# Performance work log

Measured on AMD Instinct MI355X. Metric: run time of the kernel, lower is better.

The kernel has to match this reference:

```python
import jax, jax.numpy as jnp
import numpy as np

E = 1024   # embedding_dim
H = 16     # heads
W = 1024   # lag / seq length
B = 4      # batch
D = E // H # head dim


def setup_inputs() -> dict:
    key = jax.random.key(0)
    ks = jax.random.split(key, 5)
    scale = E ** -0.5
    return {
        "x":   jax.random.normal(ks[0], (3, B, E, W), dtype=jnp.float32),
        "L_Q": jax.random.normal(ks[1], (E, E), dtype=jnp.float32) * scale,
        "L_K": jax.random.normal(ks[2], (E, E), dtype=jnp.float32) * scale,
        "L_V": jax.random.normal(ks[3], (E, E), dtype=jnp.float32) * scale,
        "M":   jax.random.normal(ks[4], (E, E), dtype=jnp.float32) * (1.0 / (2 * E)) ** 0.5,
        "b":   jnp.zeros((E, 1), dtype=jnp.float32),
    }


def reference(x, L_Q, L_K, L_V, M, b):
    # x: [3, B, E, W] channels-first; x[0]=K input, x[1]=Q input, x[2]=V input
    K = jnp.einsum('ef,bfw->bew', L_K, x[0])
    Q = jnp.einsum('ef,bfw->bew', L_Q, x[1])
    V = jnp.einsum('ef,bfw->bew', L_V, x[2])
    # reshape to [B, H, D, W]
    Kv = K.reshape(B, H, D, W)
    Qv = Q.reshape(B, H, D, W)
    Vv = V.reshape(B, H, D, W)
    # scores[b,h,q,k] = Q_v^T @ K_v
    scores = jnp.einsum('bhdq,bhdk->bhqk', Qv, Kv)
    # causal mask: -inf for q > k (strictly lower triangle), added BEFORE softmax
    q_idx = jnp.arange(W)[:, None]
    k_idx = jnp.arange(W)[None, :]
    mask = jnp.where(q_idx > k_idx, -jnp.inf, 0.0).astype(scores.dtype)
    scores = scores + mask
    # NON-STANDARD: softmax over the QUERY axis (dim=-2), then scale
    attn = jax.nn.softmax(scores, axis=-2) / (E ** 0.5)
    # V_v @ scores: [B,H,D,W] @ [B,H,W,W] -> [B,H,D,W]
    out = jnp.einsum('bhdq,bhqk->bhdk', Vv, attn).reshape(B, E, W)
    # dense: M @ out + b (dropout identity at inference)
    return jnp.einsum('oe,bew->bow', M, out) + b
```

## Files before the change

### kernel.cpp

```cpp
#include <hip/hip_runtime.h>
#include <stdint.h>
#include <math.h>

#define E_DIM 1024
#define W_DIM 1024
#define EW 1048576L

typedef _Float16 h16;
typedef __attribute__((ext_vector_type(8))) _Float16 h8;
typedef __attribute__((ext_vector_type(4))) float f4;

__device__ __forceinline__ void async_copy16(h16* lds, const h16* g) {
    __builtin_amdgcn_global_load_lds(
        (const __attribute__((address_space(1))) void*)g,
        (__attribute__((address_space(3))) void*)lds, 16, 0, 0);
}

__global__ __launch_bounds__(256) void prep(
    const float* __restrict__ x, const float* __restrict__ LK,
    const float* __restrict__ LQ, const float* __restrict__ LV,
    const float* __restrict__ Mw, h16* __restrict__ xt, h16* __restrict__ wh)
{
    __shared__ float Ts[64][65];
    const int z = blockIdx.z;
    const int t = threadIdx.x;
    if (z < 12) {
        const float* src = x + (long)z * EW;
        h16* dst = xt + (long)z * EW;
        const int e0 = blockIdx.y * 64, w0 = blockIdx.x * 64;
        const int r = t >> 4, c4 = (t & 15) * 4;
        #pragma unroll
        for (int p = 0; p < 4; ++p) {
            float4 v = *reinterpret_cast<const float4*>(src + (long)(e0 + r + p * 16) * W_DIM + w0 + c4);
            Ts[c4 + 0][r + p * 16] = v.x;
            Ts[c4 + 1][r + p * 16] = v.y;
            Ts[c4 + 2][r + p * 16] = v.z;
            Ts[c4 + 3][r + p * 16] = v.w;
        }
        __syncthreads();
        #pragma unroll
        for (int p = 0; p < 4; ++p) {
            int wr = r + p * 16;
            union { h16 h[4]; uint2 u; } o;
            o.h[0] = (h16)Ts[wr][c4 + 0];
            o.h[1] = (h16)Ts[wr][c4 + 1];
            o.h[2] = (h16)Ts[wr][c4 + 2];
            o.h[3] = (h16)Ts[wr][c4 + 3];
            *reinterpret_cast<uint2*>(dst + (long)(w0 + wr) * E_DIM + e0 + c4) = o.u;
        }
    } else {
        const float* srcs[4] = {LK, LQ, LV, Mw};
        const float* s = srcs[z - 12];
        h16* o = wh + (long)(z - 12) * EW;
        long base = ((long)(blockIdx.y * 16 + blockIdx.x)) * 1024 + t;
        #pragma unroll
        for (int k = 0; k < 4; ++k) {
            long i = base + k * 256;
            float4 v = reinterpret_cast<const float4*>(s)[i];
            union { h16 h[4]; uint2 u; } u;
            u.h[0] = (h16)v.x; u.h[1] = (h16)v.y; u.h[2] = (h16)v.z; u.h[3] = (h16)v.w;
            reinterpret_cast<uint2*>(o)[i] = u.u;
        }
    }
}

__global__ __launch_bounds__(512) void gemm_proj3(
    const h16* __restrict__ xh, const h16* __restrict__ Wts,
    h16* __restrict__ KQV)
{
    __shared__ h16 As[4][256 * 32];
    __shared__ h16 Bs[4][256 * 32];

    const int t = threadIdx.x;
    const int wave = t >> 6, lane = t & 63;
    const int quad = lane >> 4, l16 = lane & 15;
    const int mi = wave >> 2, ni = wave & 3;
    const int wm = mi * 128, wn = ni * 64;

    const int lin = (int)blockIdx.x + ((int)blockIdx.y << 2) + ((int)blockIdx.z << 4);
    const int swz = (lin & 7) * 24 + (lin >> 3);
    const int bx = swz & 3, by = (swz >> 2) & 3, zz = swz >> 4;

    const int m0 = by * 256, n0 = bx * 256;

    const int proj = zz >> 2, bz = zz & 3;
    const h16 *A, *Bt; h16* C;
    if (proj == 0)      { A = xh + bz * EW;       Bt = Wts;          C = KQV + bz * EW; }
    else if (proj == 1) { A = xh + (4 + bz) * EW; Bt = Wts + EW;     C = KQV + (4 + bz) * EW; }
    else                { A = Wts + 2 * EW;       Bt = xh + (8 + bz) * EW; C = KQV + (8 + bz) * EW; }

    f4 acc[8][4] = {};

    auto stageA = [&](int buf, int k0) {
        #pragma unroll
        for (int j = 0; j < 2; ++j) {
            int g = j * 512 + t, row = g >> 2, cg = (g & 3) ^ ((row >> 1) & 3);
            async_copy16(&As[buf][g * 8], A + (long)(m0 + row) * E_DIM + k0 + cg * 8);
        }
    };
    auto stageB = [&](int buf, int k0) {
        #pragma unroll
        for (int j = 0; j < 2; ++j) {
            int g = j * 512 + t, row = g >> 2, cg = (g & 3) ^ ((row >> 1) & 3);
            async_copy16(&Bs[buf][g * 8], Bt + (long)(n0 + row) * E_DIM + k0 + cg * 8);
        }
    };

    stageA(0, 0);  stageB(0, 0);
    stageA(1, 32); stageB(1, 32);
    stageA(2, 64); stageB(2, 64);
    asm volatile("s_waitcnt vmcnt(8)" ::: "memory");
    __builtin_amdgcn_s_barrier();

    for (int H = 0; H < 32; ++H) {
        const h16* as = As[H & 3];
        const h16* bs = Bs[H & 3];
        const int kn = (H + 3) * 32;
        const bool st = (H + 3) < 32;

        h8 bv[4], av[4];
        #pragma unroll
        for (int j = 0; j < 4; ++j) {
            int rb = wn + j * 16 + l16;
            bv[j] = *reinterpret_cast<const h8*>(&bs[(rb * 4 + (quad ^ ((rb >> 1) & 3))) * 8]);
        }
        #pragma unroll
        for (int i = 0; i < 4; ++i) {
            int ra = wm + i * 16 + l16;
            av[i] = *reinterpret_cast<const h8*>(&as[(ra * 4 + (quad ^ ((ra >> 1) & 3))) * 8]);
        }
        if (st) stageA((H + 3) & 3, kn);
        __builtin_amdgcn_s_barrier();
        __builtin_amdgcn_s_setprio(1);
        #pragma unroll
        for (int i = 0; i < 4; ++i)
            #pragma unroll
            for (int j = 0; j < 4; ++j)
                acc[i][j] = __builtin_amdgcn_mfma_f32_16x16x32_f16(av[i], bv[j], acc[i][j], 0, 0, 0);
        __builtin_amdgcn_s_setprio(0);
        __builtin_amdgcn_s_barrier();

        #pragma unroll
        for (int i = 0; i < 4; ++i) {
            int ra = wm + 64 + i * 16 + l16;
            av[i] = *reinterpret_cast<const h8*>(&as[(ra * 4 + (quad ^ ((ra >> 1) & 3))) * 8]);
        }
        if (st) stageB((H + 3) & 3, kn);
        if (H < 29)       asm volatile("s_waitcnt vmcnt(8)" ::: "memory");
        else if (H == 29) asm volatile("s_waitcnt vmcnt(4)" ::: "memory");
        else if (H == 30) asm volatile("s_waitcnt vmcnt(0)" ::: "memory");
        __builtin_amdgcn_s_barrier();
        __builtin_amdgcn_s_setprio(1);
        #pragma unroll
        for (int i = 0; i < 4; ++i)
            #pragma unroll
            for (int j = 0; j < 4; ++j)
                acc[4 + i][j] = __builtin_amdgcn_mfma_f32_16x16x32_f16(av[i], bv[j], acc[4 + i][j], 0, 0, 0);
        __builtin_amdgcn_s_setprio(0);
        __builtin_amdgcn_s_barrier();
    }

    #pragma unroll
    for (int mt = 0; mt < 8; ++mt)
        #pragma unroll
        for (int i = 0; i < 4; ++i) {
            int m = m0 + wm + mt * 16 + quad * 4 + i;
            #pragma unroll
            for (int nt = 0; nt < 4; ++nt)
                C[(long)m * W_DIM + n0 + wn + nt * 16 + l16] = (h16)acc[mt][nt][i];
        }
}

__global__ __launch_bounds__(256) void gemm_out(
    const h16* __restrict__ A, const h16* __restrict__ Bt,
    float* __restrict__ C, const float* __restrict__ bias)
{
    __shared__ h16 As[64 * 64];
    __shared__ h16 Bs[128 * 64];

    const int t = threadIdx.x;
    const int wave = t >> 6, lane = t & 63;
    const int quad = lane >> 4, l16 = lane & 15;
    const int m0 = blockIdx.y * 64, n0 = blockIdx.x * 128;
    const int wm = (wave >> 1) * 32, wn = (wave & 1) * 64;

    f4 acc[2][4] = {};

    for (int k0 = 0; k0 < 1024; k0 += 64) {
        __syncthreads();
        #pragma unroll
        for (int j = 0; j < 2; ++j) {
            int g = j * 256 + t, row = g >> 3, cg = (g & 7) ^ (row & 7);
            async_copy16(&As[g * 8], A + (long)(m0 + row) * E_DIM + k0 + cg * 8);
        }
        #pragma unroll
        for (int j = 0; j < 4; ++j) {
            int g = j * 256 + t, row = g >> 3, cg = (g & 7) ^ (row & 7);
            async_copy16(&Bs[g * 8], Bt + (long)(n0 + row) * E_DIM + k0 + cg * 8);
        }
        __syncthreads();

        h8 av[2][2], bv[4][2];
        #pragma unroll
        for (int c = 0; c < 2; ++c) {
            #pragma unroll
            for (int mt = 0; mt < 2; ++mt) {
                int r = wm + mt * 16 + l16;
                av[mt][c] = *reinterpret_cast<const h8*>(&As[(r * 8 + ((c * 4 + quad) ^ (l16 & 7))) * 8]);
            }
            #pragma unroll
            for (int nt = 0; nt < 4; ++nt) {
                int r = wn + nt * 16 + l16;
                bv[nt][c] = *reinterpret_cast<const h8*>(&Bs[(r * 8 + ((c * 4 + quad) ^ (l16 & 7))) * 8]);
            }
        }
        #pragma unroll
        for (int c = 0; c < 2; ++c)
            #pragma unroll
            for (int mt = 0; mt < 2; ++mt)
                #pragma unroll
                for (int nt = 0; nt < 4; ++nt)
                    acc[mt][nt] = __builtin_amdgcn_mfma_f32_16x16x32_f16(av[mt][c], bv[nt][c], acc[mt][nt], 0, 0, 0);
    }

    #pragma unroll
    for (int mt = 0; mt < 2; ++mt)
        #pragma unroll
        for (int i = 0; i < 4; ++i) {
            int m = m0 + wm + mt * 16 + quad * 4 + i;
            float bv_ = bias ? bias[m] : 0.f;
            #pragma unroll
            for (int nt = 0; nt < 4; ++nt) {
                int n = n0 + wn + nt * 16 + l16;
                C[(long)(n >> 10) * EW + (long)m * W_DIM + (n & 1023)] = acc[mt][nt][i] + bv_;
            }
        }
}

__global__ __launch_bounds__(512) void attn_mfma(
    const h16* __restrict__ Kt, const h16* __restrict__ Qt,
    const h16* __restrict__ V, h16* __restrict__ AoT)
{
    __shared__ h16 Qs[2][64 * 64];
    __shared__ h16 Vs[2][64 * 64];
    __shared__ h16 Ps[8][16 * 64];

    const int t = threadIdx.x, wave = t >> 6, lane = t & 63;
    const int quad = lane >> 4, l16 = lane & 15;
    const int y = blockIdx.y;
    const int b = y >> 4, h = y & 15;
    const int cxor = (y & 7) ^ (((y >> 5) & 1) ? 7 : 0);
    const int ktb = (int)blockIdx.x ^ cxor;
    const int nit = 2 * ktb + 2;
    const int kwave = ktb * 128 + wave * 16;
    const int kc = kwave + l16;

    const h16* Ktb_ = Kt + (long)b * EW + h * 64;
    const h16* Qtb  = Qt + (long)b * EW + h * 64;
    const h16* Vb   = V  + (long)b * EW + (long)(h * 64) * W_DIM;
    h16* Pw = &Ps[wave][0];

    h8 kb0 = *reinterpret_cast<const h8*>(Ktb_ + (long)kc * E_DIM + quad * 8);
    h8 kb1 = *reinterpret_cast<const h8*>(Ktb_ + (long)kc * E_DIM + 32 + quad * 8);

    {
        int row = t >> 3, cg = (t & 7) ^ (row & 7);
        async_copy16(&Qs[0][t * 8], Qtb + (long)row * E_DIM + cg * 8);
        async_copy16(&Vs[0][t * 8], Vb + (long)row * W_DIM + cg * 8);
    }

    const float L2E = 1.442695041f;
    float mr = -1e30f, ls = 0.f;
    f4 O[4] = {};

    for (int it = 0; it < nit; ++it) {
        const int q0 = it * 64;
        __syncthreads();
        if (it + 1 < nit) {
            const int nb = (it + 1) & 1, q1 = q0 + 64;
            int row = t >> 3, cg = (t & 7) ^ (row & 7);
            async_copy16(&Qs[nb][t * 8], Qtb + (long)(q1 + row) * E_DIM + cg * 8);
            async_copy16(&Vs[nb][t * 8], Vb + (long)row * W_DIM + q1 + cg * 8);
        }
        if (q0 > kwave + 15) continue;

        const h16* qs = Qs[it & 1];
        const h16* vs = Vs[it & 1];

        f4 S[4];
        __builtin_amdgcn_s_setprio(1);
        #pragma unroll
        for (int nt = 0; nt < 4; ++nt) {
            int row = nt * 16 + l16;
            h8 a0 = *reinterpret_cast<const h8*>(&qs[(row * 8 + (quad ^ (l16 & 7))) * 8]);
            h8 a1 = *reinterpret_cast<const h8*>(&qs[(row * 8 + ((4 + quad) ^ (l16 & 7))) * 8]);
            f4 s = {};
            s = __builtin_amdgcn_mfma_f32_16x16x32_f16(a0, kb0, s, 0, 0, 0);
            s = __builtin_amdgcn_mfma_f32_16x16x32_f16(a1, kb1, s, 0, 0, 0);
            S[nt] = s;
        }
        __builtin_amdgcn_s_setprio(0);

        if (it >= 2 * ktb) {
            #pragma unroll
            for (int nt = 0; nt < 4; ++nt)
                #pragma unroll
                for (int i = 0; i < 4; ++i)
                    if (q0 + nt * 16 + quad * 4 + i > kc) S[nt][i] = -1e30f;
        }

        float mx = -1e30f;
        #pragma unroll
        for (int nt = 0; nt < 4; ++nt) {
            float t0 = fmaxf(fmaxf(S[nt][0], S[nt][1]), fmaxf(S[nt][2], S[nt][3]));
            mx = fmaxf(mx, t0);
        }
        mx = fmaxf(mx, __shfl_xor(mx, 16));
        mx = fmaxf(mx, __shfl_xor(mx, 32));

        if (__any(mx - mr > 8.f)) {
            float nm = fmaxf(mr, mx);
            float al = exp2f((mr - nm) * L2E);
            mr = nm;
            ls *= al;
            #pragma unroll
            for (int dt = 0; dt < 4; ++dt)
                #pragma unroll
                for (int i = 0; i < 4; ++i) O[dt][i] *= al;
        }

        const float mc = mr * L2E;
        float tsa = 0.f, tsb = 0.f;
        #pragma unroll
        for (int nt = 0; nt < 4; ++nt)
            #pragma unroll
            for (int i = 0; i < 4; ++i) {
                float p = exp2f(fmaf(S[nt][i], L2E, -mc));
                S[nt][i] = p;
                if (i & 1) tsb += p; else tsa += p;
            }
        float ts = tsa + tsb;
        ts += __shfl_xor(ts, 16);
        ts += __shfl_xor(ts, 32);
        ls += ts;

        #pragma unroll
        for (int nt = 0; nt < 4; ++nt) {
            int sg = ((nt * 2 + (quad >> 1)) ^ (l16 & 7)) * 8 + (quad & 1) * 4;
            union { h16 hh[4]; uint2 u2; } u0;
            #pragma unroll
            for (int i = 0; i < 4; ++i) u0.hh[i] = (h16)S[nt][i];
            *reinterpret_cast<uint2*>(Pw + l16 * 64 + sg) = u0.u2;
        }
        asm volatile("" ::: "memory");

        __builtin_amdgcn_s_setprio(1);
        #pragma unroll
        for (int c = 0; c < 2; ++c) {
            int sg = ((c * 4 + quad) ^ (l16 & 7)) * 8;
            h8 pb = *reinterpret_cast<const h8*>(Pw + l16 * 64 + sg);
            #pragma unroll
            for (int dt = 0; dt < 4; ++dt) {
                int r = dt * 16 + l16;
                h8 va = *reinterpret_cast<const h8*>(&vs[(r * 8 + ((c * 4 + quad) ^ (l16 & 7))) * 8]);
                O[dt] = __builtin_amdgcn_mfma_f32_16x16x32_f16(va, pb, O[dt], 0, 0, 0);
            }
        }
        __builtin_amdgcn_s_setprio(0);
    }

    const float inv = 0.03125f / ls;
    #pragma unroll
    for (int dt = 0; dt < 4; ++dt) {
        int sg = ((dt * 2 + (quad >> 1)) ^ (l16 & 7)) * 8 + (quad & 1) * 4;
        union { h16 hh[4]; uint2 u2; } u0;
        #pragma unroll
        for (int i = 0; i < 4; ++i) u0.hh[i] = (h16)(O[dt][i] * inv);
        *reinterpret_cast<uint2*>(Pw + l16 * 64 + sg) = u0.u2;
    }
    asm volatile("" ::: "memory");
    #pragma unroll
    for (int j = 0; j < 2; ++j) {
        int sg = ((quad * 2 + j) ^ (l16 & 7)) * 8;
        uint4 vv = *reinterpret_cast<const uint4*>(Pw + l16 * 64 + sg);
        *reinterpret_cast<uint4*>(AoT + (long)b * EW + (long)(kwave + l16) * E_DIM
                                  + h * 64 + quad * 16 + j * 8) = vv;
    }
}

extern "C" void kernel_launch(void* const* d_in, const int* in_sizes, int n_in,
                              void* d_out, int out_size, void* d_ws, size_t ws_size,
                              hipStream_t stream)
{
    const float* x  = (const float*)d_in[0];
    const float* LQ = (const float*)d_in[1];
    const float* LK = (const float*)d_in[2];
    const float* LV = (const float*)d_in[3];
    const float* Mw = (const float*)d_in[4];
    const float* bb = (const float*)d_in[5];
    float* out = (float*)d_out;
    h16* ws = (h16*)d_ws;

    h16* xh  = ws;
    h16* LKh = ws + 12 * EW;
    h16* Mh  = ws + 15 * EW;
    h16* Kp  = ws + 16 * EW;
    h16* Qp  = ws + 20 * EW;
    h16* Vp  = ws + 24 * EW;
    h16* Ao  = ws + 28 * EW;

    dim3 blk(256);
    prep<<<dim3(16, 16, 16), blk, 0, stream>>>(x, LK, LQ, LV, Mw, xh, LKh);
    gemm_proj3<<<dim3(4, 4, 12), dim3(512), 0, stream>>>(xh, LKh, Kp);
    attn_mfma<<<dim3(8, 64), dim3(512), 0, stream>>>(Kp, Qp, Vp, Ao);
    gemm_out<<<dim3(32, 16), blk, 0, stream>>>(Mh, Ao, out, bb);
}
```

Before: 188.7 us.

## Stage 128-query tiles per barrier in attention and widen prep transpose stores

The attention kernel now loads two 64-row Q/V sub-tiles per pipeline stage. This halves the number of __syncthreads barriers and outer iterations, and the inner loop walks the two sub-tiles. LDS use for Q/V doubles to 64KB, which may limit occupancy, and the causal skip now works per sub-tile inside a larger stage. Separately, the prep transpose writes 16-byte fp16 stores instead of 8-byte ones to get wider global writes.

```diff
diff --git a/kernel.cpp b/kernel.cpp
--- a/kernel.cpp
+++ b/kernel.cpp
@@ -38,15 +38,14 @@
             Ts[c4 + 3][r + p * 16] = v.w;
         }
         __syncthreads();
-        #pragma unroll
-        for (int p = 0; p < 4; ++p) {
-            int wr = r + p * 16;
-            union { h16 h[4]; uint2 u; } o;
-            o.h[0] = (h16)Ts[wr][c4 + 0];
-            o.h[1] = (h16)Ts[wr][c4 + 1];
-            o.h[2] = (h16)Ts[wr][c4 + 2];
-            o.h[3] = (h16)Ts[wr][c4 + 3];
-            *reinterpret_cast<uint2*>(dst + (long)(w0 + wr) * E_DIM + e0 + c4) = o.u;
+        const int r2 = t >> 3, c8 = (t & 7) * 8;
+        #pragma unroll
+        for (int p = 0; p < 2; ++p) {
+            int wr = r2 + p * 32;
+            union { h16 h[8]; uint4 u; } o;
+            #pragma unroll
+            for (int k = 0; k < 8; ++k) o.h[k] = (h16)Ts[wr][c8 + k];
+            *reinterpret_cast<uint4*>(dst + (long)(w0 + wr) * E_DIM + e0 + c8) = o.u;
         }
     } else {
         const float* srcs[4] = {LK, LQ, LV, Mw};
@@ -241,8 +240,8 @@
     const h16* __restrict__ Kt, const h16* __restrict__ Qt,
     const h16* __restrict__ V, h16* __restrict__ AoT)
 {
-    __shared__ h16 Qs[2][64 * 64];
-    __shared__ h16 Vs[2][64 * 64];
+    __shared__ h16 Qs[2][2][64 * 64];
+    __shared__ h16 Vs[2][2][64 * 64];
     __shared__ h16 Ps[8][16 * 64];
 
     const int t = threadIdx.x, wave = t >> 6, lane = t & 63;
@@ -251,7 +250,7 @@
     const int b = y >> 4, h = y & 15;
     const int cxor = (y & 7) ^ (((y >> 5) & 1) ? 7 : 0);
     const int ktb = (int)blockIdx.x ^ cxor;
-    const int nit = 2 * ktb + 2;
+    const int nit = ktb + 1;
     const int kwave = ktb * 128 + wave * 16;
     const int kc = kwave + l16;
 
@@ -263,10 +262,11 @@
     h8 kb0 = *reinterpret_cast<const h8*>(Ktb_ + (long)kc * E_DIM + quad * 8);
     h8 kb1 = *reinterpret_cast<const h8*>(Ktb_ + (long)kc * E_DIM + 32 + quad * 8);
 
-    {
-        int row = t >> 3, cg = (t & 7) ^ (row & 7);
-        async_copy16(&Qs[0][t * 8], Qtb + (long)row * E_DIM + cg * 8);
-        async_copy16(&Vs[0][t * 8], Vb + (long)row * W_DIM + cg * 8);
+    const int srow = t >> 3, scg = (t & 7) ^ (srow & 7);
+    #pragma unroll
+    for (int hs = 0; hs < 2; ++hs) {
+        async_copy16(&Qs[0][hs][t * 8], Qtb + (long)(hs * 64 + srow) * E_DIM + scg * 8);
+        async_copy16(&Vs[0][hs][t * 8], Vb + (long)srow * W_DIM + hs * 64 + scg * 8);
     }
 
     const float L2E = 1.442695041f;
@@ -274,99 +274,106 @@
     f4 O[4] = {};
 
     for (int it = 0; it < nit; ++it) {
-        const int q0 = it * 64;
+        const int q0 = it * 128;
         __syncthreads();
         if (it + 1 < nit) {
-            const int nb = (it + 1) & 1, q1 = q0 + 64;
-            int row = t >> 3, cg = (t & 7) ^ (row & 7);
-            async_copy16(&Qs[nb][t * 8], Qtb + (long)(q1 + row) * E_DIM + cg * 8);
-            async_copy16(&Vs[nb][t * 8], Vb + (long)row * W_DIM + q1 + cg * 8);
-        }
-        if (q0 > kwave + 15) continue;
-
-        const h16* qs = Qs[it & 1];
-        const h16* vs = Vs[it & 1];
-
-        f4 S[4];
-        __builtin_amdgcn_s_setprio(1);
-        #pragma unroll
-        for (int nt = 0; nt < 4; ++nt) {
-            int row = nt * 16 + l16;
-            h8 a0 = *reinterpret_cast<const h8*>(&qs[(row * 8 + (quad ^ (l16 & 7))) * 8]);
-            h8 a1 = *reinterpret_cast<const h8*>(&qs[(row * 8 + ((4 + quad) ^ (l16 & 7))) * 8]);
-            f4 s = {};
-            s = __builtin_amdgcn_mfma_f32_16x16x32_f16(a0, kb0, s, 0, 0, 0);
-            s = __builtin_amdgcn_mfma_f32_16x16x32_f16(a1, kb1, s, 0, 0, 0);
-            S[nt] = s;
-        }
-        __builtin_amdgcn_s_setprio(0);
-
-        if (it >= 2 * ktb) {
+            const int nb = (it + 1) & 1, q1 = q0 + 128;
+            #pragma unroll
+            for (int hs = 0; hs < 2; ++hs) {
+                async_copy16(&Qs[nb][hs][t * 8], Qtb + (long)(q1 + hs * 64 + srow) * E_DIM + scg * 8);
+                async_copy16(&Vs[nb][hs][t * 8], Vb + (long)srow * W_DIM + q1 + hs * 64 + scg * 8);
+            }
+        }
+
+        for (int sub = 0; sub < 2; ++sub) {
+            const int q0s = q0 + sub * 64;
+            if (q0s > kwave + 15) continue;
+
+            const h16* qs = &Qs[it & 1][sub][0];
+            const h16* vs = &Vs[it & 1][sub][0];
+
+            f4 S[4];
+            __builtin_amdgcn_s_setprio(1);
+            #pragma unroll
+            for (int nt = 0; nt < 4; ++nt) {
+                int row = nt * 16 + l16;
+                h8 a0 = *reinterpret_cast<const h8*>(&qs[(row * 8 + (quad ^ (l16 & 7))) * 8]);
+                h8 a1 = *reinterpret_cast<const h8*>(&qs[(row * 8 + ((4 + quad) ^ (l16 & 7))) * 8]);
+                f4 s = {};
+                s = __builtin_amdgcn_mfma_f32_16x16x32_f16(a0, kb0, s, 0, 0, 0);
+                s = __builtin_amdgcn_mfma_f32_16x16x32_f16(a1, kb1, s, 0, 0, 0);
+                S[nt] = s;
+            }
+            __builtin_amdgcn_s_setprio(0);
+
+            if (2 * it + sub >= 2 * ktb) {
+                #pragma unroll
+                for (int nt = 0; nt < 4; ++nt)
+                    #pragma unroll
+                    for (int i = 0; i < 4; ++i)
+                        if (q0s + nt * 16 + quad * 4 + i > kc) S[nt][i] = -1e30f;
+            }
+
+            float mx = -1e30f;
+            #pragma unroll
+            for (int nt = 0; nt < 4; ++nt) {
+                float t0 = fmaxf(fmaxf(S[nt][0], S[nt][1]), fmaxf(S[nt][2], S[nt][3]));
+                mx = fmaxf(mx, t0);
+            }
+            mx = fmaxf(mx, __shfl_xor(mx, 16));
+            mx = fmaxf(mx, __shfl_xor(mx, 32));
+
+            if (__any(mx - mr > 8.f)) {
+                float nm = fmaxf(mr, mx);
+                float al = exp2f((mr - nm) * L2E);
+                mr = nm;
+                ls *= al;
+                #pragma unroll
+                for (int dt = 0; dt < 4; ++dt)
+                    #pragma unroll
+                    for (int i = 0; i < 4; ++i) O[dt][i] *= al;
+            }
+
+            const float mc = mr * L2E;
+            float tsa = 0.f, tsb = 0.f;
             #pragma unroll
             for (int nt = 0; nt < 4; ++nt)
                 #pragma unroll
-                for (int i = 0; i < 4; ++i)
-                    if (q0 + nt * 16 + quad * 4 + i > kc) S[nt][i] = -1e30f;
-        }
-
-        float mx = -1e30f;
-        #pragma unroll
-        for (int nt = 0; nt < 4; ++nt) {
-            float t0 = fmaxf(fmaxf(S[nt][0], S[nt][1]), fmaxf(S[nt][2], S[nt][3]));
-            mx = fmaxf(mx, t0);
-        }
-        mx = fmaxf(mx, __shfl_xor(mx, 16));
-        mx = fmaxf(mx, __shfl_xor(mx, 32));
-
-        if (__any(mx - mr > 8.f)) {
-            float nm = fmaxf(mr, mx);
-            float al = exp2f((mr - nm) * L2E);
-            mr = nm;
-            ls *= al;
-            #pragma unroll
-            for (int dt = 0; dt < 4; ++dt)
-                #pragma unroll
-                for (int i = 0; i < 4; ++i) O[dt][i] *= al;
-        }
-
-        const float mc = mr * L2E;
-        float tsa = 0.f, tsb = 0.f;
-        #pragma unroll
-        for (int nt = 0; nt < 4; ++nt)
-            #pragma unroll
-            for (int i = 0; i < 4; ++i) {
-                float p = exp2f(fmaf(S[nt][i], L2E, -mc));
-                S[nt][i] = p;
-                if (i & 1) tsb += p; else tsa += p;
-            }
-        float ts = tsa + tsb;
-        ts += __shfl_xor(ts, 16);
-        ts += __shfl_xor(ts, 32);
-        ls += ts;
-
-        #pragma unroll
-        for (int nt = 0; nt < 4; ++nt) {
-            int sg = ((nt * 2 + (quad >> 1)) ^ (l16 & 7)) * 8 + (quad & 1) * 4;
-            union { h16 hh[4]; uint2 u2; } u0;
-            #pragma unroll
-            for (int i = 0; i < 4; ++i) u0.hh[i] = (h16)S[nt][i];
-            *reinterpret_cast<uint2*>(Pw + l16 * 64 + sg) = u0.u2;
-        }
-        asm volatile("" ::: "memory");
-
-        __builtin_amdgcn_s_setprio(1);
-        #pragma unroll
-        for (int c = 0; c < 2; ++c) {
-            int sg = ((c * 4 + quad) ^ (l16 & 7)) * 8;
-            h8 pb = *reinterpret_cast<const h8*>(Pw + l16 * 64 + sg);
-            #pragma unroll
-            for (int dt = 0; dt < 4; ++dt) {
-                int r = dt * 16 + l16;
-                h8 va = *reinterpret_cast<const h8*>(&vs[(r * 8 + ((c * 4 + quad) ^ (l16 & 7))) * 8]);
-                O[dt] = __builtin_amdgcn_mfma_f32_16x16x32_f16(va, pb, O[dt], 0, 0, 0);
-            }
-        }
-        __builtin_amdgcn_s_setprio(0);
+                for (int i = 0; i < 4; ++i) {
+                    float p = exp2f(fmaf(S[nt][i], L2E, -mc));
+                    S[nt][i] = p;
+                    if (i & 1) tsb += p; else tsa += p;
+                }
+            float ts = tsa + tsb;
+            ts += __shfl_xor(ts, 16);
+            ts += __shfl_xor(ts, 32);
+            ls += ts;
+
+            #pragma unroll
+            for (int nt = 0; nt < 4; ++nt) {
+                int sg = ((nt * 2 + (quad >> 1)) ^ (l16 & 7)) * 8 + (quad & 1) * 4;
+                union { h16 hh[4]; uint2 u2; } u0;
+                #pragma unroll
+                for (int i = 0; i < 4; ++i) u0.hh[i] = (h16)S[nt][i];
+                *reinterpret_cast<uint2*>(Pw + l16 * 64 + sg) = u0.u2;
+            }
+            asm volatile("" ::: "memory");
+
+            __builtin_amdgcn_s_setprio(1);
+            #pragma unroll
+            for (int c = 0; c < 2; ++c) {
+                int sg = ((c * 4 + quad) ^ (l16 & 7)) * 8;
+                h8 pb = *reinterpret_cast<const h8*>(Pw + l16 * 64 + sg);
+                #pragma unroll
+                for (int dt = 0; dt < 4; ++dt) {
+                    int r = dt * 16 + l16;
+                    h8 va = *reinterpret_cast<const h8*>(&vs[(r * 8 + ((c * 4 + quad) ^ (l16 & 7))) * 8]);
+                    O[dt] = __builtin_amdgcn_mfma_f32_16x16x32_f16(va, pb, O[dt], 0, 0, 0);
+                }
+            }
+            __builtin_amdgcn_s_setprio(0);
+            asm volatile("" ::: "memory");
+        }
     }
 
     const float inv = 0.03125f / ls;
```

Measured after the change: 186.4 us (median of 2 runs). Within noise of the previous version (-1.2%).
